# Kernel tuning notes

Hardware: AMD Instinct MI355X
Metric: run time of the kernel (lower is better)

Reference implementation:

```python
import jax, jax.numpy as jnp
import numpy as np

B, C, D = 4, 2048, 1024
DCONV, DMAMBA, K, DSTATE = 512, 512, 4, 16
FFN = 2560


def setup_inputs() -> dict:
    key = jax.random.key(0)
    ks = jax.random.split(key, 16)
    n = lambda k, shape, s=1.0: jax.random.normal(k, shape, jnp.float32) * s
    inv = lambda f: 1.0 / float(np.sqrt(f))
    return {
        "x": n(ks[0], (B, C, D)),
        "velocity": n(ks[1], (B, C, D), 0.1),
        "v_hat_chunk": n(ks[2], (B, C, D)),
        "delta_W": n(ks[3], (FFN, D), 0.01),
        "pre_norm_w": jnp.ones((D,), jnp.float32),
        "ffn_norm_w": jnp.ones((D,), jnp.float32),
        "conv_in_w": n(ks[4], (D, 2 * DCONV), inv(D)),
        "conv_kernel_w": n(ks[5], (K, 1, DCONV), inv(K)),
        "ssm_in_w": n(ks[6], (D, 2 * DMAMBA), inv(D)),
        "ssm_dt_w": n(ks[7], (D, DMAMBA), inv(D)),
        "ssm_dt_b": jnp.full((DMAMBA,), -4.0, jnp.float32),
        "ssm_A_log": jnp.tile(jnp.log(jnp.arange(1.0, DSTATE + 1, dtype=jnp.float32)), (DMAMBA, 1)),
        "ssm_B_w": n(ks[8], (D, DSTATE), inv(D)),
        "ssm_C_w": n(ks[9], (D, DSTATE), inv(D)),
        "ssm_D": jnp.ones((DMAMBA,), jnp.float32),
        "out_proj_w": n(ks[10], (D, D), inv(D)),
        "log_beta": jnp.array(0.0, jnp.float32),  # sigmoid -> beta=0.5
        "ffn_gate_up_w": n(ks[11], (D, 2 * FFN), inv(D)),
        "ffn_down_w": n(ks[12], (FFN, D), inv(FFN)),
        "ffn_target_w": n(ks[13], (D, FFN), inv(D)),
        "log_gamma": jnp.array(0.0, jnp.float32),
        "log_eta": jnp.array(-4.0, jnp.float32),
    }


def _rms(x, w, eps=1e-6):
    return x * jax.lax.rsqrt(jnp.mean(x * x, axis=-1, keepdims=True) + eps) * w


def _gated_conv(xn, w_in, kernel):
    # proj -> split gate/value, depthwise causal conv on value, silu-gate
    g, v = jnp.split(xn @ w_in, 2, axis=-1)  # (B,C,DCONV) each
    v = jax.lax.conv_general_dilated(
        v, kernel, window_strides=(1,), padding=[(K - 1, 0)],
        dimension_numbers=("NWC", "WIO", "NWC"), feature_group_count=DCONV)
    return jax.nn.silu(g) * v


def _ssm(xn, w_in, w_dt, dt_b, A_log, w_B, w_C, Dp):
    # Mamba-style selective SISO scan
    u, z = jnp.split(xn @ w_in, 2, axis=-1)          # (B,C,DMAMBA)
    dt = jax.nn.softplus(xn @ w_dt + dt_b)            # (B,C,DMAMBA)
    A = -jnp.exp(A_log)                               # (DMAMBA,DSTATE)
    Bs = xn @ w_B                                     # (B,C,DSTATE)
    Cs = xn @ w_C                                     # (B,C,DSTATE)
    dA = jnp.exp(dt[..., None] * A)                   # (B,C,DMAMBA,DSTATE)
    dBu = (dt * u)[..., None] * Bs[:, :, None, :]     # (B,C,DMAMBA,DSTATE)

    def step(h, inputs):
        dA_t, dBu_t, C_t = inputs
        h = dA_t * h + dBu_t                          # (B,DMAMBA,DSTATE)
        return h, jnp.einsum("bds,bs->bd", h, C_t)

    xs = (jnp.moveaxis(dA, 1, 0), jnp.moveaxis(dBu, 1, 0), jnp.moveaxis(Cs, 1, 0))
    _, ys = jax.lax.scan(step, jnp.zeros((B, DMAMBA, DSTATE), xn.dtype), xs)
    y = jnp.moveaxis(ys, 0, 1) + Dp * u               # (B,C,DMAMBA)
    return y * jax.nn.silu(z)


def reference(x, velocity, v_hat_chunk, delta_W, pre_norm_w, ffn_norm_w,
              conv_in_w, conv_kernel_w, ssm_in_w, ssm_dt_w, ssm_dt_b, ssm_A_log,
              ssm_B_w, ssm_C_w, ssm_D, out_proj_w, log_beta, ffn_gate_up_w,
              ffn_down_w, ffn_target_w, log_gamma, log_eta):
    xn = _rms(x, pre_norm_w)
    conv_out = _gated_conv(xn, conv_in_w, conv_kernel_w)
    ssm_out = _ssm(xn, ssm_in_w, ssm_dt_w, ssm_dt_b, ssm_A_log, ssm_B_w, ssm_C_w, ssm_D)
    mixed = jnp.concatenate([conv_out, ssm_out], axis=-1) @ out_proj_w
    # momentum residual
    velocity = jax.nn.sigmoid(log_beta) * velocity + mixed
    x = x + velocity
    # Living SwiGLU
    ffn_in = _rms(x, ffn_norm_w)
    gate, up = jnp.split(ffn_in @ ffn_gate_up_w, 2, axis=-1)
    z = jax.nn.silu(gate) * up                        # (B,C,FFN)
    out = z @ ffn_down_w + z @ delta_W                # fast-weight augmented down proj
    v_hat_proj = v_hat_chunk @ ffn_target_w           # (B,C,FFN)
    update = jnp.einsum("bcf,bcd->fd", v_hat_proj, ffn_in) / x.shape[0]
    new_delta_W = jax.nn.sigmoid(log_gamma) * delta_W + jax.nn.softplus(log_eta) * update
    x = x + out
    return (x, velocity, new_delta_W)
```

## Files before the change

kernel.cpp:

```cpp
#include <hip/hip_runtime.h>
#include <stdint.h>
#include <stddef.h>

#define B_ 4
#define C_ 2048
#define D_ 1024
#define FFN_ 2560
#define ROWS_ 8192

typedef unsigned short u16;
typedef short bf16x8 __attribute__((ext_vector_type(8)));
typedef float f32x4 __attribute__((ext_vector_type(4)));

__device__ __forceinline__ float bf2f(u16 x){ union { unsigned u; float f; } v; v.u = ((unsigned)x)<<16; return v.f; }
__device__ __forceinline__ u16 f2bf(float f){ union { float f; unsigned u; } v; v.f = f; unsigned r = v.u + 0x7fffu + ((v.u>>16)&1u); return (u16)(r>>16); }
__device__ __forceinline__ float sigm_(float x){ return 1.f/(1.f+__expf(-x)); }
__device__ __forceinline__ float silu_(float x){ return x/(1.f+__expf(-x)); }
__device__ __forceinline__ float softplus_(float x){ return (x>15.f)? x : log1pf(__expf(x)); }

__device__ __forceinline__ void async16(u16* lds_base, const u16* g){
  __builtin_amdgcn_global_load_lds((const __attribute__((address_space(1))) unsigned int*)g,
                                   (__attribute__((address_space(3))) unsigned int*)lds_base,
                                   16, 0, 0);
}

#define EPI_INTRANS   0
#define EPI_MOM       1
#define EPI_SWIGLU    2
#define EPI_DOWNDELTA 3

template<int EPI>
__global__ __launch_bounds__(256)
void gemm128(const u16* __restrict__ A, const u16* __restrict__ Bt,
             int M, int N, int K, int ksplit,
             float* __restrict__ f0, float* __restrict__ f1,
             const float* __restrict__ c0, const float* __restrict__ c1, const float* __restrict__ c2,
             u16* __restrict__ h0, u16* __restrict__ h1, u16* __restrict__ h2,
             const u16* __restrict__ a2, const u16* __restrict__ b2)
{
  __shared__ u16 smem[16384];
  u16* As = smem;
  u16* Bs = smem + 8192;
  const int tid  = threadIdx.x;
  const int wave = tid>>6, lane = tid&63;

  int bx = blockIdx.x;
  bool alt = false;
  if constexpr (EPI == EPI_INTRANS){
    if (bx >= 21){ alt = true; bx -= 21; A = a2; Bt = b2; }
  }
  if constexpr (EPI == EPI_DOWNDELTA){
    if (bx >= 8){
      alt = true; bx -= 8;
      if ((int)blockIdx.y >= 20) return;
      A = a2; Bt = b2; K = 8192; ksplit = 2048;
    } else {
      if ((int)blockIdx.z >= 2) return;
    }
  }
  const int bm = blockIdx.y*128, bn = bx*128;

  const int lr8  = lane>>3;
  const int kswz = ((lane&7) ^ lr8)*8;
  const u16* aG[4]; const u16* bG[4]; u16* aL[4]; u16* bL[4];
  #pragma unroll
  for (int q=0;q<4;q++){
    const int r = wave*32 + q*8 + lr8;
    aG[q] = A  + (size_t)(bm + r)*K + kswz;
    bG[q] = Bt + (size_t)(bn + r)*K + kswz;
    aL[q] = As + (wave*32 + q*8)*64;
    bL[q] = Bs + (wave*32 + q*8)*64;
  }
  const int wr = wave>>1, wc = wave&1;
  const int mrow = lane&15, quad = lane>>4;
  const int swz8 = (mrow&7);

  f32x4 acc[4][4];
  #pragma unroll
  for (int i=0;i<4;i++)
    #pragma unroll
    for (int j=0;j<4;j++) acc[i][j] = (f32x4){0.f,0.f,0.f,0.f};

  const int kbeg = blockIdx.z * ksplit;
  const int kend = kbeg + ksplit;
  for (int k0=kbeg; k0<kend; k0+=64){
    __syncthreads();
    #pragma unroll
    for (int q=0;q<4;q++) async16(aL[q], aG[q] + k0);
    #pragma unroll
    for (int q=0;q<4;q++) async16(bL[q], bG[q] + k0);
    __syncthreads();
    #pragma unroll
    for (int kk=0; kk<64; kk+=32){
      bf16x8 af[4], bfv[4];
      const int gq = (kk>>3) + quad;
      const int pos = (gq ^ swz8)*8;
      #pragma unroll
      for (int i=0;i<4;i++) af[i]  = *(const bf16x8*)(As + (wr*64+i*16+mrow)*64 + pos);
      #pragma unroll
      for (int j=0;j<4;j++) bfv[j] = *(const bf16x8*)(Bs + (wc*64+j*16+mrow)*64 + pos);
      #pragma unroll
      for (int i=0;i<4;i++)
        #pragma unroll
        for (int j=0;j<4;j++)
          acc[i][j] = __builtin_amdgcn_mfma_f32_16x16x32_bf16(af[i], bfv[j], acc[i][j], 0,0,0);
    }
  }

  if constexpr (EPI == EPI_INTRANS){
    if (alt){
      __syncthreads();
      #pragma unroll
      for (int h=0; h<4; h++){
        const int hw = h>>1, j0 = (h&1)*2;
        if (wc == hw){
          #pragma unroll
          for (int i=0;i<4;i++){
            const int rbase = wr*64 + i*16 + quad*4;
            #pragma unroll
            for (int jj=0;jj<2;jj++){
              const int j = j0+jj;
              const int cl = jj*16 + mrow;
              f32x4 v = acc[i][j];
              #pragma unroll
              for (int t=0;t<4;t++) smem[cl*132 + rbase + t] = f2bf(v[t]);
            }
          }
        }
        __syncthreads();
        {
          const int cl2 = tid>>3, m0 = (tid&7)*16;
          const int col = bn + h*32 + cl2;
          const ushort4* s4 = (const ushort4*)(smem + cl2*132 + m0);
          ushort4* d4 = (ushort4*)(h2 + (size_t)col*8192 + bm + m0);
          #pragma unroll
          for (int q=0;q<4;q++) d4[q] = s4[q];
        }
        __syncthreads();
      }
    } else {
      #pragma unroll
      for (int i=0;i<4;i++){
        const int row0 = bm + wr*64 + i*16 + quad*4;
        #pragma unroll
        for (int j=0;j<4;j++){
          const int col = bn + wc*64 + j*16 + mrow;
          f32x4 v = acc[i][j];
          if (col < 1024){
            #pragma unroll
            for (int t=0;t<4;t++) h0[(size_t)(row0+t)*1024 + col] = f2bf(v[t]);
          } else if (col < 2048){
            #pragma unroll
            for (int t=0;t<4;t++) h1[(size_t)(row0+t)*1024 + (col-1024)] = f2bf(v[t]);
          } else if (col < 2560){
            const float b = c0[col-2048];
            #pragma unroll
            for (int t=0;t<4;t++) f0[(size_t)(row0+t)*512 + (col-2048)] = softplus_(v[t]+b);
          } else {
            const int cl = col - 2560;
            if (cl < 32){
              #pragma unroll
              for (int t=0;t<4;t++) f1[(size_t)(row0+t)*32 + cl] = v[t];
            }
          }
        }
      }
    }
  } else if constexpr (EPI == EPI_MOM){
    const float beta = sigm_(c2[0]);
    #pragma unroll
    for (int i=0;i<4;i++){
      const int row0 = bm + wr*64 + i*16 + quad*4;
      #pragma unroll
      for (int j=0;j<4;j++){
        const int col = bn + wc*64 + j*16 + mrow;
        f32x4 v = acc[i][j];
        #pragma unroll
        for (int t=0;t<4;t++){
          size_t idx = (size_t)(row0+t)*1024 + col;
          float vel = beta*c0[idx] + v[t];
          f0[idx] = vel;
          f1[idx] = c1[idx] + vel;
        }
      }
    }
  } else if constexpr (EPI == EPI_SWIGLU){
    #pragma unroll
    for (int i=0;i<4;i++){
      const int row0 = bm + wr*64 + i*16 + quad*4;
      #pragma unroll
      for (int jp=0;jp<4;jp+=2){
        f32x4 g = acc[i][jp];
        f32x4 u = acc[i][jp+1];
        const int o = (((bn + wc*64 + jp*16)>>5)<<4) + mrow;
        #pragma unroll
        for (int t=0;t<4;t++) h0[(size_t)(row0+t)*2560 + o] = f2bf(silu_(g[t])*u[t]);
      }
    }
  } else if constexpr (EPI == EPI_DOWNDELTA){
    #pragma unroll
    for (int i=0;i<4;i++){
      const int row0 = bm + wr*64 + i*16 + quad*4;
      #pragma unroll
      for (int j=0;j<4;j++){
        const int col = bn + wc*64 + j*16 + mrow;
        f32x4 v = acc[i][j];
        if (!alt){
          #pragma unroll
          for (int t=0;t<4;t++) atomicAdd(&f0[(size_t)(row0+t)*1024 + col], v[t]);
        } else {
          const float e = softplus_(c2[0])*0.25f;
          #pragma unroll
          for (int t=0;t<4;t++) atomicAdd(&f1[(size_t)(row0+t)*1024 + col], e*v[t]);
        }
      }
    }
  }
}

__global__ void prep_transposes(const float* __restrict__ conv_in_w, const float* __restrict__ ssm_in_w,
                                const float* __restrict__ ssm_dt_w, const float* __restrict__ out_proj_w,
                                const float* __restrict__ ffn_tgt_w, const float* __restrict__ gate_up_w,
                                u16* __restrict__ Wti, u16* __restrict__ out_proj_t,
                                u16* __restrict__ target_t, u16* __restrict__ gate_up_t)
{
  const int z = blockIdx.z;
  const float* W; u16* Wt; int N; bool gu = false;
  switch(z){
    case 0: W=conv_in_w;  Wt=Wti;                       N=1024; break;
    case 1: W=ssm_in_w;   Wt=Wti + (size_t)1024*1024;   N=1024; break;
    case 2: W=ssm_dt_w;   Wt=Wti + (size_t)2048*1024;   N=512;  break;
    case 3: W=out_proj_w; Wt=out_proj_t;                N=1024; break;
    case 4: W=ffn_tgt_w;  Wt=target_t;                  N=2560; break;
    default: W=gate_up_w; Wt=gate_up_t;                 N=5120; gu=true; break;
  }
  const int c0 = blockIdx.x*32, r0 = blockIdx.y*32;
  if (c0 >= N) return;
  __shared__ float tile[32][33];
  const int tx = threadIdx.x, ty = threadIdx.y;
  #pragma unroll
  for (int i=0;i<4;i++) tile[ty+8*i][tx] = W[(size_t)(r0+ty+8*i)*N + c0+tx];
  __syncthreads();
  #pragma unroll
  for (int i=0;i<4;i++){
    const int c = c0+ty+8*i;
    int n;
    if (gu){
      if (c < 2560) n = ((c>>4)<<5) | (c&15);
      else { int o = c-2560; n = ((o>>4)<<5) | 16 | (o&15); }
    } else n = c;
    Wt[(size_t)n*1024 + r0+tx] = f2bf(tile[tx][ty+8*i]);
  }
}

__global__ void weff_transpose(const float* __restrict__ Wa, const float* __restrict__ Wb, u16* __restrict__ Wt)
{
  __shared__ float tile[32][33];
  const int tx = threadIdx.x, ty = threadIdx.y;
  const int c0 = blockIdx.x*32, r0 = blockIdx.y*32;
  #pragma unroll
  for (int i=0;i<4;i++){
    size_t idx = (size_t)(r0+ty+8*i)*1024 + c0+tx;
    tile[ty+8*i][tx] = Wa[idx] + Wb[idx];
  }
  __syncthreads();
  #pragma unroll
  for (int i=0;i<4;i++) Wt[(size_t)(c0+ty+8*i)*2560 + r0+tx] = f2bf(tile[tx][ty+8*i]);
}

__global__ void transpose_bf16(const u16* __restrict__ in, u16* __restrict__ out, int R, int Cc)
{
  __shared__ u16 tile[32][33];
  const int tx = threadIdx.x, ty = threadIdx.y;
  const int c0 = blockIdx.x*32, r0 = blockIdx.y*32;
  #pragma unroll
  for (int i=0;i<4;i++) tile[ty+8*i][tx] = in[(size_t)(r0+ty+8*i)*Cc + c0+tx];
  __syncthreads();
  #pragma unroll
  for (int i=0;i<4;i++) out[(size_t)(c0+ty+8*i)*R + r0+tx] = tile[tx][ty+8*i];
}

__global__ void cvt_bf16x4(const float* __restrict__ in, u16* __restrict__ out, int n4)
{
  int i = blockIdx.x*256 + threadIdx.x;
  if (i < n4){
    float4 v = ((const float4*)in)[i];
    ushort4 p; p.x=f2bf(v.x); p.y=f2bf(v.y); p.z=f2bf(v.z); p.w=f2bf(v.w);
    ((ushort4*)out)[i] = p;
  }
}

__global__ void prep_small(const float* __restrict__ dW, const float* __restrict__ lg,
                           const float* __restrict__ Bw, const float* __restrict__ Cw,
                           const float* __restrict__ A_log,
                           float* __restrict__ out_delta, u16* __restrict__ bc_dst,
                           float* __restrict__ A_tab)
{
  const int blk = blockIdx.x, tid = threadIdx.x;
  if (blk < 2560){
    int i = blk*256 + tid;
    float g = sigm_(lg[0]);
    float4 v = ((const float4*)dW)[i];
    float4 r; r.x=g*v.x; r.y=g*v.y; r.z=g*v.z; r.w=g*v.w;
    ((float4*)out_delta)[i] = r;
  } else if (blk < 3072){
    int i = (blk-2560)*256 + tid;
    int r = i >> 10, k = i & 1023;
    float v = 0.f;
    if (r < 16) v = Bw[k*16 + r];
    else if (r < 32) v = Cw[k*16 + (r-16)];
    bc_dst[(size_t)r*1024 + k] = f2bf(v);
  } else {
    int i = (blk-3072)*256 + tid;
    if (i < 512*16) A_tab[i] = -__expf(A_log[i]);
  }
}

__global__ __launch_bounds__(256) void rmsnorm_k(const float* __restrict__ x, const float* __restrict__ w, u16* __restrict__ out)
{
  const int row = blockIdx.x, tid = threadIdx.x;
  float4 v = ((const float4*)(x + (size_t)row*1024))[tid];
  float s = v.x*v.x + v.y*v.y + v.z*v.z + v.w*v.w;
  #pragma unroll
  for (int o=32;o>0;o>>=1) s += __shfl_down(s, o);
  __shared__ float red[4];
  const int wave = tid>>6, lane = tid&63;
  if (lane==0) red[wave] = s;
  __syncthreads();
  float tot = red[0]+red[1]+red[2]+red[3];
  float sc = rsqrtf(tot*(1.f/1024.f) + 1e-6f);
  float4 wv = ((const float4*)w)[tid];
  ushort4 p; p.x=f2bf(v.x*sc*wv.x); p.y=f2bf(v.y*sc*wv.y); p.z=f2bf(v.z*sc*wv.z); p.w=f2bf(v.w*sc*wv.w);
  ((ushort4*)(out + (size_t)row*1024))[tid] = p;
}

__global__ __launch_bounds__(256) void conv_k(const u16* __restrict__ P1, const float* __restrict__ kw, u16* __restrict__ mixed)
{
  const int idx = blockIdx.x*256 + threadIdx.x;
  const int c = idx & 511;
  const int t = (idx>>9) & 2047;
  const int b = idx >> 20;
  const size_t rowb = (size_t)b*2048;
  float g = bf2f(P1[(rowb+t)*1024 + c]);
  float acc = 0.f;
  #pragma unroll
  for (int k=0;k<4;k++){
    int tt = t-3+k;
    if (tt>=0) acc += bf2f(P1[(rowb+tt)*1024 + 512 + c]) * kw[k*512+c];
  }
  mixed[(rowb+t)*1024 + c] = f2bf(silu_(g)*acc);
}

#define NCH_ 64
#define CHL_ 32
__global__ __launch_bounds__(256) void scan_p1(const float* __restrict__ dt, const u16* __restrict__ P2,
                                               const float* __restrict__ BCs, const float* __restrict__ A_tab,
                                               float* __restrict__ hend, float* __restrict__ aprod)
{
  const int d = blockIdx.x*256 + threadIdx.x;
  const int ch = blockIdx.y, b = blockIdx.z;
  float Ar[16], h[16], ap[16];
  #pragma unroll
  for (int s=0;s<16;s++){ Ar[s] = A_tab[d*16+s]; h[s]=0.f; ap[s]=1.f; }
  const int t0 = ch*CHL_;
  for (int t=0;t<CHL_;t++){
    size_t row = (size_t)b*2048 + t0 + t;
    float dtv = dt[row*512 + d];
    float u = bf2f(P2[row*1024 + d]);
    float du = dtv*u;
    const float* bs = BCs + row*32;
    #pragma unroll
    for (int s=0;s<16;s++){
      float dA = __expf(dtv*Ar[s]);
      h[s] = dA*h[s] + du*bs[s];
      ap[s] *= dA;
    }
  }
  size_t o = ((size_t)((b*512+d)*NCH_ + ch))*16;
  #pragma unroll
  for (int s=0;s<16;s++){ hend[o+s]=h[s]; aprod[o+s]=ap[s]; }
}

__global__ __launch_bounds__(256) void scan_p2(float* __restrict__ hend, const float* __restrict__ aprod)
{
  const int g = blockIdx.x*256 + threadIdx.x;
  const int s = g & 15, bd = g >> 4;
  float h = 0.f;
  for (int ch=0; ch<NCH_; ch++){
    size_t o = ((size_t)(bd*NCH_+ch))*16 + s;
    float he = hend[o], ap = aprod[o];
    hend[o] = h;
    h = ap*h + he;
  }
}

__global__ __launch_bounds__(256) void scan_p3(const float* __restrict__ dt, const u16* __restrict__ P2,
                                               const float* __restrict__ BCs, const float* __restrict__ A_tab,
                                               const float* __restrict__ hin, const float* __restrict__ Dp,
                                               u16* __restrict__ mixed)
{
  const int d = blockIdx.x*256 + threadIdx.x;
  const int ch = blockIdx.y, b = blockIdx.z;
  float Ar[16], h[16];
  size_t o = ((size_t)((b*512+d)*NCH_ + ch))*16;
  #pragma unroll
  for (int s=0;s<16;s++){ Ar[s] = A_tab[d*16+s]; h[s] = hin[o+s]; }
  const float Dd = Dp[d];
  const int t0 = ch*CHL_;
  for (int t=0;t<CHL_;t++){
    size_t row = (size_t)b*2048 + t0 + t;
    float dtv = dt[row*512 + d];
    float u = bf2f(P2[row*1024 + d]);
    float zv = bf2f(P2[row*1024 + 512 + d]);
    float du = dtv*u;
    const float* bs = BCs + row*32;
    const float* cs = bs + 16;
    float y = 0.f;
    #pragma unroll
    for (int s=0;s<16;s++){
      float dA = __expf(dtv*Ar[s]);
      h[s] = dA*h[s] + du*bs[s];
      y += h[s]*cs[s];
    }
    float outv = (y + Dd*u)*silu_(zv);
    mixed[row*1024 + 512 + d] = f2bf(outv);
  }
}

extern "C" void kernel_launch(void* const* d_in, const int* in_sizes, int n_in,
                              void* d_out, int out_size, void* d_ws, size_t ws_size,
                              hipStream_t stream)
{
  const float* x          = (const float*)d_in[0];
  const float* velocity   = (const float*)d_in[1];
  const float* v_hat      = (const float*)d_in[2];
  const float* delta_W    = (const float*)d_in[3];
  const float* pre_norm_w = (const float*)d_in[4];
  const float* ffn_norm_w = (const float*)d_in[5];
  const float* conv_in_w  = (const float*)d_in[6];
  const float* conv_kw    = (const float*)d_in[7];
  const float* ssm_in_w   = (const float*)d_in[8];
  const float* ssm_dt_w   = (const float*)d_in[9];
  const float* ssm_dt_b   = (const float*)d_in[10];
  const float* ssm_A_log  = (const float*)d_in[11];
  const float* ssm_B_w    = (const float*)d_in[12];
  const float* ssm_C_w    = (const float*)d_in[13];
  const float* ssm_D      = (const float*)d_in[14];
  const float* out_proj_w = (const float*)d_in[15];
  const float* log_beta   = (const float*)d_in[16];
  const float* gate_up_w  = (const float*)d_in[17];
  const float* ffn_down_w = (const float*)d_in[18];
  const float* ffn_tgt_w  = (const float*)d_in[19];
  const float* log_gamma  = (const float*)d_in[20];
  const float* log_eta    = (const float*)d_in[21];

  float* out_x     = (float*)d_out;
  float* out_vel   = out_x + (size_t)ROWS_*D_;
  float* out_delta = out_vel + (size_t)ROWS_*D_;

  char* wsp = (char*)d_ws;
  size_t off = 0;
  auto alloc = [&](size_t bytes)->char*{ char* p = wsp + off; off += (bytes + 255) & ~(size_t)255; return p; };

  u16* Wti        = (u16*)alloc((size_t)2688*1024*2);
  u16* out_proj_t = (u16*)alloc((size_t)1024*1024*2);
  u16* gate_up_t  = (u16*)alloc((size_t)5120*1024*2);
  u16* target_t   = (u16*)alloc((size_t)2560*1024*2);
  u16* weff_t     = (u16*)alloc((size_t)1024*2560*2);
  float* A_tab    = (float*)alloc((size_t)512*16*4);
  u16* xn         = (u16*)alloc((size_t)ROWS_*1024*2);
  u16* P1         = (u16*)alloc((size_t)ROWS_*1024*2);
  u16* P2         = (u16*)alloc((size_t)ROWS_*1024*2);
  float* dtbuf    = (float*)alloc((size_t)ROWS_*512*4);
  float* BCs      = (float*)alloc((size_t)ROWS_*32*4);
  float* hend     = (float*)alloc((size_t)4*512*NCH_*16*4);
  float* aprod    = (float*)alloc((size_t)4*512*NCH_*16*4);
  u16* mixed      = (u16*)alloc((size_t)ROWS_*1024*2);
  u16* ffn_in     = (u16*)alloc((size_t)ROWS_*1024*2);
  u16* zbuf       = (u16*)alloc((size_t)ROWS_*2560*2);
  u16* T1t        = (u16*)alloc((size_t)2560*ROWS_*2);
  u16* ffn_inT    = xn;
  u16* vhat_bf    = mixed;

  dim3 tb(32,8);
  prep_transposes<<<dim3(160,32,6), tb, 0, stream>>>(conv_in_w, ssm_in_w, ssm_dt_w, out_proj_w,
      ffn_tgt_w, gate_up_w, Wti, out_proj_t, target_t, gate_up_t);
  weff_transpose<<<dim3(32,80), tb, 0, stream>>>(ffn_down_w, delta_W, weff_t);
  prep_small<<<3104, 256, 0, stream>>>(delta_W, log_gamma, ssm_B_w, ssm_C_w, ssm_A_log,
      out_delta, Wti + (size_t)2560*1024, A_tab);
  cvt_bf16x4<<<8192, 256, 0, stream>>>(v_hat, vhat_bf, ROWS_*1024/4);

  rmsnorm_k<<<ROWS_, 256, 0, stream>>>(x, pre_norm_w, xn);
  gemm128<EPI_INTRANS><<<dim3(41,64), 256, 0, stream>>>(xn, Wti, ROWS_,2688,1024,1024,
      dtbuf, BCs, ssm_dt_b, nullptr, nullptr, P1, P2, T1t, vhat_bf, target_t);

  conv_k<<<16384, 256, 0, stream>>>(P1, conv_kw, mixed);
  scan_p1<<<dim3(2,NCH_,4), 256, 0, stream>>>(dtbuf, P2, BCs, A_tab, hend, aprod);
  scan_p2<<<128, 256, 0, stream>>>(hend, aprod);
  scan_p3<<<dim3(2,NCH_,4), 256, 0, stream>>>(dtbuf, P2, BCs, A_tab, hend, ssm_D, mixed);

  gemm128<EPI_MOM><<<dim3(8,64), 256, 0, stream>>>(mixed, out_proj_t, ROWS_,1024,1024,1024,
      out_vel, out_x, velocity, x, log_beta, nullptr, nullptr, nullptr, nullptr, nullptr);

  rmsnorm_k<<<ROWS_, 256, 0, stream>>>(out_x, ffn_norm_w, ffn_in);
  transpose_bf16<<<dim3(32,256), tb, 0, stream>>>(ffn_in, ffn_inT, ROWS_, 1024);

  gemm128<EPI_SWIGLU><<<dim3(40,64), 256, 0, stream>>>(ffn_in, gate_up_t, ROWS_,5120,1024,1024,
      nullptr,nullptr,nullptr,nullptr,nullptr, zbuf, nullptr, nullptr, nullptr, nullptr);

  gemm128<EPI_DOWNDELTA><<<dim3(16,64,4), 256, 0, stream>>>(zbuf, weff_t, ROWS_,1024,2560,1280,
      out_x, out_delta, nullptr, nullptr, log_eta, nullptr, nullptr, nullptr, T1t, ffn_inT);
}
```

Measured before the change: 877.5 us.

## Split fused down/delta GEMM into separate launches with non-atomic down epilogue

Replaces the single combined down-projection plus delta-update GEMM launch with two kernels. The down projection now uses the full K with no split, so it does a plain read-add-write into x instead of atomic adds. The delta update runs as its own launch with an 8-way K split and keeps atomic adds. This removes atomic traffic and wasted early-exit blocks on the down path, at the cost of an extra launch and less parallelism for the down GEMM (512 blocks).

```diff
diff --git a/kernel.cpp b/kernel.cpp
--- a/kernel.cpp
+++ b/kernel.cpp
@@ -24,10 +24,11 @@
                                    16, 0, 0);
 }
 
-#define EPI_INTRANS   0
-#define EPI_MOM       1
-#define EPI_SWIGLU    2
-#define EPI_DOWNDELTA 3
+#define EPI_INTRANS 0
+#define EPI_MOM     1
+#define EPI_SWIGLU  2
+#define EPI_DOWN    3
+#define EPI_DELTA   4
 
 template<int EPI>
 __global__ __launch_bounds__(256)
@@ -48,15 +49,6 @@
   bool alt = false;
   if constexpr (EPI == EPI_INTRANS){
     if (bx >= 21){ alt = true; bx -= 21; A = a2; Bt = b2; }
-  }
-  if constexpr (EPI == EPI_DOWNDELTA){
-    if (bx >= 8){
-      alt = true; bx -= 8;
-      if ((int)blockIdx.y >= 20) return;
-      A = a2; Bt = b2; K = 8192; ksplit = 2048;
-    } else {
-      if ((int)blockIdx.z >= 2) return;
-    }
   }
   const int bm = blockIdx.y*128, bn = bx*128;
 
@@ -197,7 +189,7 @@
         for (int t=0;t<4;t++) h0[(size_t)(row0+t)*2560 + o] = f2bf(silu_(g[t])*u[t]);
       }
     }
-  } else if constexpr (EPI == EPI_DOWNDELTA){
+  } else if constexpr (EPI == EPI_DOWN){
     #pragma unroll
     for (int i=0;i<4;i++){
       const int row0 = bm + wr*64 + i*16 + quad*4;
@@ -205,14 +197,24 @@
       for (int j=0;j<4;j++){
         const int col = bn + wc*64 + j*16 + mrow;
         f32x4 v = acc[i][j];
-        if (!alt){
-          #pragma unroll
-          for (int t=0;t<4;t++) atomicAdd(&f0[(size_t)(row0+t)*1024 + col], v[t]);
-        } else {
-          const float e = softplus_(c2[0])*0.25f;
-          #pragma unroll
-          for (int t=0;t<4;t++) atomicAdd(&f1[(size_t)(row0+t)*1024 + col], e*v[t]);
+        #pragma unroll
+        for (int t=0;t<4;t++){
+          size_t idx = (size_t)(row0+t)*1024 + col;
+          f0[idx] = f0[idx] + v[t];
         }
+      }
+    }
+  } else if constexpr (EPI == EPI_DELTA){
+    const float e = softplus_(c2[0])*0.25f;
+    #pragma unroll
+    for (int i=0;i<4;i++){
+      const int row0 = bm + wr*64 + i*16 + quad*4;
+      #pragma unroll
+      for (int j=0;j<4;j++){
+        const int col = bn + wc*64 + j*16 + mrow;
+        f32x4 v = acc[i][j];
+        #pragma unroll
+        for (int t=0;t<4;t++) atomicAdd(&f0[(size_t)(row0+t)*1024 + col], e*v[t]);
       }
     }
   }
@@ -508,6 +510,9 @@
   gemm128<EPI_SWIGLU><<<dim3(40,64), 256, 0, stream>>>(ffn_in, gate_up_t, ROWS_,5120,1024,1024,
       nullptr,nullptr,nullptr,nullptr,nullptr, zbuf, nullptr, nullptr, nullptr, nullptr);
 
-  gemm128<EPI_DOWNDELTA><<<dim3(16,64,4), 256, 0, stream>>>(zbuf, weff_t, ROWS_,1024,2560,1280,
-      out_x, out_delta, nullptr, nullptr, log_eta, nullptr, nullptr, nullptr, T1t, ffn_inT);
-}
+  gemm128<EPI_DOWN><<<dim3(8,64), 256, 0, stream>>>(zbuf, weff_t, ROWS_,1024,2560,2560,
+      out_x, nullptr, nullptr, nullptr, nullptr, nullptr, nullptr, nullptr, nullptr, nullptr);
+
+  gemm128<EPI_DELTA><<<dim3(8,20,8), 256, 0, stream>>>(T1t, ffn_inT, 2560,1024,ROWS_,1024,
+      out_delta, nullptr, nullptr, nullptr, log_eta, nullptr, nullptr, nullptr, nullptr, nullptr);
+}
```

Result: faster. 823.1 us (-6.2%).
